# Kernel optimization log

Hardware: AMD Instinct MI355X
Metric: run time of the kernel (lower is better)

## Reference

```python
import jax, jax.numpy as jnp
import numpy as np

B, N, C, H, NC = 8, 4096, 512, 256, 1000
GRID = 64  # N = GRID*GRID unique positions
LN_EPS = 1e-5


def setup_inputs() -> dict:
    key = jax.random.key(0)
    ks = jax.random.split(key, 10)
    # unique integer grid positions, same for every batch element (original order)
    i = jnp.arange(N)
    base = jnp.stack([i % GRID, i // GRID], axis=-1).astype(jnp.float32)  # [N,2]
    pos_org = jnp.broadcast_to(base, (B, N, 2))
    # per-batch random permutation -> shuffled positions (as the backbone would emit)
    perm = jax.vmap(lambda k: jax.random.permutation(k, N))(jax.random.split(ks[0], B))  # [B,N]
    pos_shuffled = jnp.take_along_axis(pos_org, perm[..., None], axis=1)
    s = 0.02
    return {
        "feat": jax.random.normal(ks[1], (B, N, C), jnp.float32),
        "prev_out": jax.random.normal(ks[2], (B, N, C), jnp.float32),
        "pos_org": pos_org,
        "pos_shuffled": pos_shuffled,
        "proj_W": jax.random.normal(ks[3], (C, C), jnp.float32) * s,
        "proj_b": jnp.zeros((C,), jnp.float32),
        "ln_g": jnp.ones((C,), jnp.float32),
        "ln_b": jnp.zeros((C,), jnp.float32),
        "W1": jax.random.normal(ks[4], (H, C), jnp.float32) * s,
        "b1": jnp.zeros((H,), jnp.float32),
        "W2": jax.random.normal(ks[5], (H, H), jnp.float32) * s,
        "b2": jnp.zeros((H,), jnp.float32),
        "W3": jax.random.normal(ks[6], (NC, H), jnp.float32) * s,
        "b3": jnp.zeros((NC,), jnp.float32),
    }


def _layernorm(x, g, b):
    x32 = x.astype(jnp.float32)
    mu = x32.mean(-1, keepdims=True)
    var = ((x32 - mu) ** 2).mean(-1, keepdims=True)
    return (x32 - mu) * jax.lax.rsqrt(var + LN_EPS) * g + b


def reference(feat, prev_out, pos_org, pos_shuffled, proj_W, proj_b,
              ln_g, ln_b, W1, b1, W2, b2, W3, b3):
    # find_pos_org_order: L1 cdist [B,N,N] + argmin over shuffled axis
    dists = jnp.abs(pos_org[:, :, None, :] - pos_shuffled[:, None, :, :]).sum(-1)
    pos_indices = jnp.argmin(dists, axis=2)  # [B,N]
    # batched gather: feat[b_, pos_indices]
    g = jnp.take_along_axis(feat, pos_indices[..., None], axis=1)  # [B,N,C]
    # fused proj -> layernorm (in fp32) -> cast back -> residual add
    proj = jnp.einsum('bnc,dc->bnd', g, proj_W) + proj_b
    out_feat = prev_out + _layernorm(proj, ln_g, ln_b).astype(feat.dtype)
    # mean-pool over tokens, 3-layer MLP head with relu on first two layers
    pooled = out_feat.mean(1)  # [B,C]
    h = jax.nn.relu(pooled @ W1.T + b1)
    h = jax.nn.relu(h @ W2.T + b2)
    return h @ W3.T + b3  # [B, num_classes]
```

## Files before the change

kernel.cpp:

```cpp
#include <hip/hip_runtime.h>
#include <stdint.h>

#define B_ 8
#define N_ 4096
#define C_ 512
#define H_ 256
#define NC_ 1000

typedef float v4f __attribute__((ext_vector_type(4)));
typedef short v8s __attribute__((ext_vector_type(8)));
typedef unsigned short ushort_t;

__device__ __forceinline__ uint32_t f2bf1(float f) {
    uint32_t u = __float_as_uint(f);
    return (u + 0x7FFFu + ((u >> 16) & 1u)) >> 16;
}
__device__ __forceinline__ uint32_t pk2(float lo, float hi) {
#if __has_builtin(__builtin_amdgcn_cvt_pk_bf16_f32)
    auto r = __builtin_amdgcn_cvt_pk_bf16_f32(lo, hi);
    return __builtin_bit_cast(uint32_t, r);
#else
    return f2bf1(lo) | (f2bf1(hi) << 16);
#endif
}

__global__ void prep_kernel(const float* __restrict__ ps, const float* __restrict__ W,
                            int* __restrict__ inv, ushort_t* __restrict__ Wfrag,
                            float* __restrict__ pooled) {
    int blk = blockIdx.x, t = threadIdx.x;
    if (blk == 0) {
        float4 z = {0.f, 0.f, 0.f, 0.f};
#pragma unroll
        for (int i = 0; i < 4; i++) ((float4*)pooled)[t * 4 + i] = z;
    }
    if (blk < 128) {
        int gid = blk * 256 + t;
        float2 p = ((const float2*)ps)[gid];
        int key = (int)(p.x + 0.5f) + 64 * (int)(p.y + 0.5f);
        int b = gid >> 12;
        inv[(b << 12) + key] = gid & 4095;
    } else {
        int i = (blk - 128) * 256 + t;
        int d = i >> 6, kb = (i >> 2) & 15, q = i & 3;
        const float4* src = (const float4*)(W + d * C_ + kb * 32 + q * 8);
        float4 v0 = src[0], v1 = src[1];
        uint4 pk;
        pk.x = pk2(v0.x, v0.y); pk.y = pk2(v0.z, v0.w);
        pk.z = pk2(v1.x, v1.y); pk.w = pk2(v1.z, v1.w);
        ((uint4*)Wfrag)[((d >> 4) * 16 + kb) * 64 + q * 16 + (d & 15)] = pk;
    }
}

__global__ __launch_bounds__(512, 4)
void gemm_ln_pool(const float* __restrict__ feat, const float* __restrict__ prev,
                  const int* __restrict__ inv, const ushort_t* __restrict__ Wfrag,
                  const float* __restrict__ pb, const float* __restrict__ lg,
                  const float* __restrict__ lb, float* __restrict__ pooled) {
    __shared__ v8s Abuf[4096];
    __shared__ float RowS[64], RowQ[64], ColS[512];

    const int bid = blockIdx.x;
    const int t = threadIdx.x;

    if (bid % 3 == 2) {
        const int p = bid / 3;
        const int b = p >> 5;
        const int r0 = (p & 31) << 7;
        const float* psrc = prev + ((size_t)(b * N_ + r0) * C_) + t;
        float s0 = 0.f, s1 = 0.f, s2 = 0.f, s3 = 0.f;
#pragma unroll 4
        for (int r = 0; r < 128; r += 4) {
            s0 += psrc[(r + 0) * C_];
            s1 += psrc[(r + 1) * C_];
            s2 += psrc[(r + 2) * C_];
            s3 += psrc[(r + 3) * C_];
        }
        atomicAdd(&pooled[b * C_ + t], (s0 + s1) + (s2 + s3));
        return;
    }

    const int gix = (bid / 3) * 2 + (bid % 3);
    const int b = gix >> 6;
    const int row0 = (gix & 63) << 6;
    const int wv = t >> 6, lane = t & 63, c = lane & 15, q = lane >> 4;

    if (t < 64) { RowS[t] = 0.f; RowQ[t] = 0.f; }

    const int arow = t >> 3;
    const int acol8 = t & 7;
    const int grow = inv[(b << 12) + row0 + arow];
    const float* asrc = feat + ((size_t)(b * N_ + grow) * C_);
#pragma unroll 4
    for (int s = 0; s < 8; s++) {
        const int chunk = s * 8 + acol8;
        float4 f0 = ((const float4*)asrc)[chunk * 2];
        float4 f1 = ((const float4*)asrc)[chunk * 2 + 1];
        uint4 pk;
        pk.x = pk2(f0.x, f0.y); pk.y = pk2(f0.z, f0.w);
        pk.z = pk2(f1.x, f1.y); pk.w = pk2(f1.z, f1.w);
        ((uint4*)Abuf)[arow * 64 + (chunk ^ (arow & 7))] = pk;
    }

    const ushort_t* fb[4];
#pragma unroll
    for (int nt = 0; nt < 4; nt++)
        fb[nt] = Wfrag + (wv * 4 + nt) * 8192 + lane * 8;

    v4f acc[4][4];
    const v4f vzero = {0.f, 0.f, 0.f, 0.f};
#pragma unroll
    for (int mt = 0; mt < 4; mt++)
#pragma unroll
        for (int nt = 0; nt < 4; nt++) acc[mt][nt] = vzero;

    __syncthreads();

#pragma unroll 2
    for (int kb = 0; kb < 16; kb++) {
        v8s af[4], bf[4];
#pragma unroll
        for (int nt = 0; nt < 4; nt++)
            bf[nt] = *((const v8s*)(fb[nt] + kb * 512));
#pragma unroll
        for (int mt = 0; mt < 4; mt++)
            af[mt] = Abuf[(mt * 16 + c) * 64 + ((kb * 4 + q) ^ (c & 7))];
#pragma unroll
        for (int mt = 0; mt < 4; mt++)
#pragma unroll
            for (int nt = 0; nt < 4; nt++)
                acc[mt][nt] = __builtin_amdgcn_mfma_f32_16x16x32_bf16(
                    af[mt], bf[nt], acc[mt][nt], 0, 0, 0);
    }

    float pb4[4], lg4[4], lb4[4];
#pragma unroll
    for (int nt = 0; nt < 4; nt++) {
        int n = wv * 64 + nt * 16 + c;
        pb4[nt] = pb[n]; lg4[nt] = lg[n]; lb4[nt] = lb[n];
    }
#pragma unroll
    for (int mt = 0; mt < 4; mt++) {
#pragma unroll
        for (int reg = 0; reg < 4; reg++) {
            float s1 = 0.f, s2 = 0.f;
#pragma unroll
            for (int nt = 0; nt < 4; nt++) {
                float v = acc[mt][nt][reg] + pb4[nt];
                acc[mt][nt][reg] = v;
                s1 += v; s2 += v * v;
            }
#pragma unroll
            for (int d = 1; d < 16; d <<= 1) {
                s1 += __shfl_xor(s1, d);
                s2 += __shfl_xor(s2, d);
            }
            if (c == 0) {
                int r = mt * 16 + q * 4 + reg;
                atomicAdd(&RowS[r], s1);
                atomicAdd(&RowQ[r], s2);
            }
        }
    }
    __syncthreads();
    if (t < 64) {
        float mu = RowS[t] * (1.f / C_);
        float var = RowQ[t] * (1.f / C_) - mu * mu;
        RowS[t] = mu;
        RowQ[t] = rsqrtf(var + 1e-5f);
    }
    __syncthreads();
    float col[4] = {0.f, 0.f, 0.f, 0.f};
#pragma unroll
    for (int mt = 0; mt < 4; mt++) {
#pragma unroll
        for (int reg = 0; reg < 4; reg++) {
            int r = mt * 16 + q * 4 + reg;
            float mu = RowS[r], rs = RowQ[r];
#pragma unroll
            for (int nt = 0; nt < 4; nt++)
                col[nt] += (acc[mt][nt][reg] - mu) * rs * lg4[nt] + lb4[nt];
        }
    }
#pragma unroll
    for (int nt = 0; nt < 4; nt++) {
        col[nt] += __shfl_xor(col[nt], 16);
        col[nt] += __shfl_xor(col[nt], 32);
    }
    if (lane < 16) {
#pragma unroll
        for (int nt = 0; nt < 4; nt++) ColS[wv * 64 + nt * 16 + c] = col[nt];
    }
    __syncthreads();
    atomicAdd(&pooled[b * C_ + t], ColS[t]);
}

__global__ __launch_bounds__(256)
void head_kernel(const float* __restrict__ pooled,
                 const float* __restrict__ W1, const float* __restrict__ b1,
                 const float* __restrict__ W2, const float* __restrict__ b2,
                 const float* __restrict__ W3, const float* __restrict__ b3,
                 float* __restrict__ out) {
    __shared__ __align__(16) float P[512];
    __shared__ __align__(16) float H1[256];
    __shared__ __align__(16) float H2[256];
    const int t = threadIdx.x, wv = t >> 6, lane = t & 63;
    const int b = blockIdx.x / 25;
    const int slice = blockIdx.x % 25;

    P[t] = pooled[b * C_ + t] * (1.f / 4096.f);
    P[t + 256] = pooled[b * C_ + t + 256] * (1.f / 4096.f);
    __syncthreads();

    {
        const float4* wr = (const float4*)(W1 + t * C_);
        float s = 0.f;
#pragma unroll 8
        for (int k = 0; k < 128; k++) {
            float4 w = wr[k];
            float4 p = ((const float4*)P)[k];
            s += w.x * p.x + w.y * p.y + w.z * p.z + w.w * p.w;
        }
        H1[t] = fmaxf(s + b1[t], 0.f);
    }
    __syncthreads();

    {
        const float4* wr = (const float4*)(W2 + t * H_);
        float s = 0.f;
#pragma unroll 8
        for (int k = 0; k < 64; k++) {
            float4 w = wr[k];
            float4 p = ((const float4*)H1)[k];
            s += w.x * p.x + w.y * p.y + w.z * p.z + w.w * p.w;
        }
        H2[t] = fmaxf(s + b2[t], 0.f);
    }
    __syncthreads();

#pragma unroll
    for (int jj = 0; jj < 10; jj++) {
        const int o = slice * 40 + jj * 4 + wv;
        float4 w = ((const float4*)(W3 + o * H_))[lane];
        float4 p = ((const float4*)H2)[lane];
        float s = w.x * p.x + w.y * p.y + w.z * p.z + w.w * p.w;
#pragma unroll
        for (int d = 1; d < 64; d <<= 1) s += __shfl_xor(s, d);
        if (lane == 0) out[b * NC_ + o] = s + b3[o];
    }
}

extern "C" void kernel_launch(void* const* d_in, const int* in_sizes, int n_in,
                              void* d_out, int out_size, void* d_ws, size_t ws_size,
                              hipStream_t stream) {
    const float* feat  = (const float*)d_in[0];
    const float* prev  = (const float*)d_in[1];
    const float* ps    = (const float*)d_in[3];
    const float* projW = (const float*)d_in[4];
    const float* pb    = (const float*)d_in[5];
    const float* lg    = (const float*)d_in[6];
    const float* lb    = (const float*)d_in[7];
    const float* W1    = (const float*)d_in[8];
    const float* b1    = (const float*)d_in[9];
    const float* W2    = (const float*)d_in[10];
    const float* b2    = (const float*)d_in[11];
    const float* W3    = (const float*)d_in[12];
    const float* b3    = (const float*)d_in[13];
    float* out = (float*)d_out;

    char* ws = (char*)d_ws;
    ushort_t* Wfrag = (ushort_t*)ws;
    int* inv        = (int*)(ws + 524288);
    float* pooled   = (float*)(ws + 655360);

    prep_kernel<<<256, 256, 0, stream>>>(ps, projW, inv, Wfrag, pooled);
    gemm_ln_pool<<<768, 512, 0, stream>>>(feat, prev, inv, Wfrag,
                                          pb, lg, lb, pooled);
    head_kernel<<<200, 256, 0, stream>>>(pooled, W1, b1, W2, b2, W3, b3, out);
}
```

Before: 219.3 us.

## Split prev_out pooling into separate kernel and drop shared-memory atomics

Moves the prev_out mean-pool reduction out of the fused GEMM/LayerNorm kernel into its own kernel, which runs 1024 blocks with 32 rows each and 16-deep independent loads. The GEMM kernel then uses a simple 512-block grid. It also issues all gathered feat loads before any bf16 conversion to raise memory-level parallelism. Per-row LayerNorm partial sums now go into per-wave shared slots that are summed afterwards, replacing LDS atomics. The costs are an extra kernel launch and serialising the two phases, which previously overlapped inside one grid.

```diff
diff --git a/kernel.cpp b/kernel.cpp
--- a/kernel.cpp
+++ b/kernel.cpp
@@ -51,54 +51,58 @@
     }
 }
 
+__global__ __launch_bounds__(512)
+void prev_pool(const float* __restrict__ prev, float* __restrict__ pooled) {
+    const int t = threadIdx.x;
+    const int b = blockIdx.x >> 7;
+    const int r0 = (blockIdx.x & 127) << 5;
+    const float* p = prev + ((size_t)(b * N_ + r0)) * C_ + t;
+    float sum = 0.f;
+#pragma unroll
+    for (int g = 0; g < 2; g++) {
+        float a[16];
+#pragma unroll
+        for (int j = 0; j < 16; j++) a[j] = p[(g * 16 + j) * C_];
+        float s = 0.f;
+#pragma unroll
+        for (int j = 0; j < 16; j++) s += a[j];
+        sum += s;
+    }
+    atomicAdd(&pooled[b * C_ + t], sum);
+}
+
 __global__ __launch_bounds__(512, 4)
-void gemm_ln_pool(const float* __restrict__ feat, const float* __restrict__ prev,
+void gemm_ln_pool(const float* __restrict__ feat,
                   const int* __restrict__ inv, const ushort_t* __restrict__ Wfrag,
                   const float* __restrict__ pb, const float* __restrict__ lg,
                   const float* __restrict__ lb, float* __restrict__ pooled) {
     __shared__ v8s Abuf[4096];
+    __shared__ float RowP[2][8][64];
     __shared__ float RowS[64], RowQ[64], ColS[512];
 
-    const int bid = blockIdx.x;
     const int t = threadIdx.x;
-
-    if (bid % 3 == 2) {
-        const int p = bid / 3;
-        const int b = p >> 5;
-        const int r0 = (p & 31) << 7;
-        const float* psrc = prev + ((size_t)(b * N_ + r0) * C_) + t;
-        float s0 = 0.f, s1 = 0.f, s2 = 0.f, s3 = 0.f;
-#pragma unroll 4
-        for (int r = 0; r < 128; r += 4) {
-            s0 += psrc[(r + 0) * C_];
-            s1 += psrc[(r + 1) * C_];
-            s2 += psrc[(r + 2) * C_];
-            s3 += psrc[(r + 3) * C_];
-        }
-        atomicAdd(&pooled[b * C_ + t], (s0 + s1) + (s2 + s3));
-        return;
-    }
-
-    const int gix = (bid / 3) * 2 + (bid % 3);
-    const int b = gix >> 6;
-    const int row0 = (gix & 63) << 6;
+    const int b = blockIdx.x >> 6;
+    const int row0 = (blockIdx.x & 63) << 6;
     const int wv = t >> 6, lane = t & 63, c = lane & 15, q = lane >> 4;
-
-    if (t < 64) { RowS[t] = 0.f; RowQ[t] = 0.f; }
 
     const int arow = t >> 3;
     const int acol8 = t & 7;
     const int grow = inv[(b << 12) + row0 + arow];
-    const float* asrc = feat + ((size_t)(b * N_ + grow) * C_);
-#pragma unroll 4
+    const float4* s4 = (const float4*)(feat + ((size_t)(b * N_ + grow) * C_));
+    float4 e[8], o[8];
+#pragma unroll
     for (int s = 0; s < 8; s++) {
-        const int chunk = s * 8 + acol8;
-        float4 f0 = ((const float4*)asrc)[chunk * 2];
-        float4 f1 = ((const float4*)asrc)[chunk * 2 + 1];
+        const int ch = s * 8 + acol8;
+        e[s] = s4[ch * 2];
+        o[s] = s4[ch * 2 + 1];
+    }
+#pragma unroll
+    for (int s = 0; s < 8; s++) {
+        const int ch = s * 8 + acol8;
         uint4 pk;
-        pk.x = pk2(f0.x, f0.y); pk.y = pk2(f0.z, f0.w);
-        pk.z = pk2(f1.x, f1.y); pk.w = pk2(f1.z, f1.w);
-        ((uint4*)Abuf)[arow * 64 + (chunk ^ (arow & 7))] = pk;
+        pk.x = pk2(e[s].x, e[s].y); pk.y = pk2(e[s].z, e[s].w);
+        pk.z = pk2(o[s].x, o[s].y); pk.w = pk2(o[s].z, o[s].w);
+        ((uint4*)Abuf)[arow * 64 + (ch ^ (arow & 7))] = pk;
     }
 
     const ushort_t* fb[4];
@@ -156,15 +160,18 @@
             }
             if (c == 0) {
                 int r = mt * 16 + q * 4 + reg;
-                atomicAdd(&RowS[r], s1);
-                atomicAdd(&RowQ[r], s2);
+                RowP[0][wv][r] = s1;
+                RowP[1][wv][r] = s2;
             }
         }
     }
     __syncthreads();
     if (t < 64) {
-        float mu = RowS[t] * (1.f / C_);
-        float var = RowQ[t] * (1.f / C_) - mu * mu;
+        float s1 = 0.f, s2 = 0.f;
+#pragma unroll
+        for (int w = 0; w < 8; w++) { s1 += RowP[0][w][t]; s2 += RowP[1][w][t]; }
+        float mu = s1 * (1.f / C_);
+        float var = s2 * (1.f / C_) - mu * mu;
         RowS[t] = mu;
         RowQ[t] = rsqrtf(var + 1e-5f);
     }
@@ -273,7 +280,7 @@
     float* pooled   = (float*)(ws + 655360);
 
     prep_kernel<<<256, 256, 0, stream>>>(ps, projW, inv, Wfrag, pooled);
-    gemm_ln_pool<<<768, 512, 0, stream>>>(feat, prev, inv, Wfrag,
-                                          pb, lg, lb, pooled);
+    prev_pool<<<1024, 512, 0, stream>>>(prev, pooled);
+    gemm_ln_pool<<<512, 512, 0, stream>>>(feat, inv, Wfrag, pb, lg, lb, pooled);
     head_kernel<<<200, 256, 0, stream>>>(pooled, W1, b1, W2, b2, W3, b3, out);
 }
```

After: 224.5 us. +2.4%, slower.
